# Optimization experiments

Hardware: AMD Instinct MI355X
Metric: run time of the kernel (lower is better)

Reference implementation:

```python
import jax, jax.numpy as jnp
import numpy as np

D_MODEL = 1024
N_HEADS = 16
D_K = D_MODEL // N_HEADS  # 64
D_FF = 2688
THETA = 10000.0
EPS = 1e-5
B, S = 2, 2048


def _rmsnorm(x, w):
    xf = x.astype(jnp.float32)
    ms = jnp.mean(xf * xf, axis=-1, keepdims=True)
    return (xf * w * jax.lax.rsqrt(ms + EPS)).astype(x.dtype)


def _rope(x, cos, sin):
    # x: [B, S, H, D_K]; cos/sin: [S, D_K//2]
    xe = x[..., 0::2]
    xo = x[..., 1::2]
    c = cos[None, :, None, :]
    s = sin[None, :, None, :]
    re = xe * c - xo * s
    ro = xe * s + xo * c
    # interleave back to even/odd layout
    return jnp.stack([re, ro], axis=-1).reshape(x.shape)


def setup_inputs() -> dict:
    key = jax.random.key(0)
    ks = jax.random.split(key, 12)
    sc = 0.02  # keep activations numerically sane (stand-in for trunc_normal init)
    return {
        "x": jax.random.normal(ks[0], (B, S, D_MODEL), dtype=jnp.float32),
        "ln1_w": jax.random.normal(ks[1], (D_MODEL,), dtype=jnp.float32) * sc + 1.0,
        "q_w": jax.random.normal(ks[2], (D_MODEL, D_MODEL), dtype=jnp.float32) * sc,
        "k_w": jax.random.normal(ks[3], (D_MODEL, D_MODEL), dtype=jnp.float32) * sc,
        "v_w": jax.random.normal(ks[4], (D_MODEL, D_MODEL), dtype=jnp.float32) * sc,
        "o_w": jax.random.normal(ks[5], (D_MODEL, D_MODEL), dtype=jnp.float32) * sc,
        "ln2_w": jax.random.normal(ks[6], (D_MODEL,), dtype=jnp.float32) * sc + 1.0,
        "w1_w": jax.random.normal(ks[7], (D_FF, D_MODEL), dtype=jnp.float32) * sc,
        "w3_w": jax.random.normal(ks[8], (D_FF, D_MODEL), dtype=jnp.float32) * sc,
        "w2_w": jax.random.normal(ks[9], (D_MODEL, D_FF), dtype=jnp.float32) * sc,
        "token_positions": jnp.arange(S, dtype=jnp.int32),
    }


def reference(x, ln1_w, q_w, k_w, v_w, o_w, ln2_w, w1_w, w3_w, w2_w, token_positions):
    b, s, _ = x.shape
    # --- pre-norm attention sublayer ---
    h = _rmsnorm(x, ln1_w)
    Q = (h @ q_w.T).reshape(b, s, N_HEADS, D_K)
    K = (h @ k_w.T).reshape(b, s, N_HEADS, D_K)
    V = (h @ v_w.T).reshape(b, s, N_HEADS, D_K)

    # RoPE tables from token positions
    pos = token_positions.astype(jnp.float32)                      # [S]
    kk = jnp.arange(D_K // 2, dtype=jnp.float32)
    inv_freq = THETA ** (-2.0 * kk / D_K)                          # [D_K/2]
    ang = pos[:, None] * inv_freq[None, :]                          # [S, D_K/2]
    cos, sin = jnp.cos(ang), jnp.sin(ang)

    Qr = _rope(Q, cos, sin)
    Kr = _rope(K, cos, sin)

    scale = 1.0 / jnp.sqrt(jnp.float32(D_K))
    scores = jnp.einsum("bqhd,bkhd->bhqk", Qr, Kr) * scale          # [B,H,S,S]
    causal = jnp.tril(jnp.ones((s, s), dtype=bool))
    scores = jnp.where(causal[None, None], scores, jnp.float32(-10000.0))
    attn = jax.nn.softmax(scores, axis=-1)
    ctx = jnp.einsum("bhqk,bkhd->bqhd", attn, V).reshape(b, s, D_MODEL)
    x1 = x + ctx @ o_w.T

    # --- pre-norm SwiGLU FFN sublayer ---
    h2 = _rmsnorm(x1, ln2_w)
    g = h2 @ w1_w.T                                                 # [B,S,D_FF]
    u = h2 @ w3_w.T
    ffn = (g * jax.nn.sigmoid(g) * u) @ w2_w.T
    return x1 + ffn
```

## Files before the change

kernel.cpp:

```cpp
#include <hip/hip_runtime.h>
#include <cstdint>

#define DM   1024
#define NH   16
#define DK   64
#define DFF  2688
#define SEQ  2048
#define BB   2
#define MTOT (BB*SEQ)

typedef __attribute__((ext_vector_type(8))) short short8;
typedef __attribute__((ext_vector_type(4))) float f32x4;

typedef const __attribute__((address_space(1))) void* gaddr_t;
typedef __attribute__((address_space(3))) void* laddr_t;
#define GLOAD_LDS16(g, l) __builtin_amdgcn_global_load_lds((gaddr_t)(g), (laddr_t)(l), 16, 0, 0)
#define MFMA16(a, b, c) __builtin_amdgcn_mfma_f32_16x16x32_bf16((a), (b), (c), 0, 0, 0)
#define WAIT_LDS() __builtin_amdgcn_s_waitcnt(0xc07f)

#define VMCNT(n) asm volatile("s_waitcnt vmcnt(" #n ")" ::: "memory")
#define BAR() do { asm volatile("" ::: "memory"); \
                   __builtin_amdgcn_s_barrier();  \
                   asm volatile("" ::: "memory"); } while (0)

__device__ __forceinline__ float bf2f(unsigned short u) {
    union { unsigned int i; float f; } v; v.i = ((unsigned int)u) << 16; return v.f;
}
__device__ __forceinline__ unsigned short f2bf(float f) {
    union { float f; unsigned int i; } v; v.f = f;
    unsigned int r = v.i + 0x7fffu + ((v.i >> 16) & 1u);
    return (unsigned short)(r >> 16);
}
__device__ __forceinline__ unsigned long long pack4bf(float a, float b, float c, float d) {
    return (unsigned long long)f2bf(a) | ((unsigned long long)f2bf(b) << 16)
         | ((unsigned long long)f2bf(c) << 32) | ((unsigned long long)f2bf(d) << 48);
}

__global__ __launch_bounds__(256)
void prep_k(const float* __restrict__ q_w, const float* __restrict__ k_w,
            const float* __restrict__ v_w, const float* __restrict__ o_w,
            const float* __restrict__ w1_w, const float* __restrict__ w3_w,
            const float* __restrict__ w2_w,
            unsigned short* __restrict__ Wqkv, unsigned short* __restrict__ Wo,
            unsigned short* __restrict__ W13, unsigned short* __restrict__ W2) {
    const int blk = blockIdx.x;
    const float* src; unsigned short* dst; int cols, rmul, roff, i;
    if (blk < 4096) {
        const int rr = blk >> 10;
        i = (blk & 1023) * 256 + threadIdx.x;
        cols = 1024; rmul = 1;
        if (rr == 0)      { src = q_w; dst = Wqkv; roff = 0; }
        else if (rr == 1) { src = k_w; dst = Wqkv; roff = 1024; }
        else if (rr == 2) { src = v_w; dst = Wqkv; roff = 2048; }
        else              { src = o_w; dst = Wo;   roff = 0; }
    } else if (blk < 6784) {
        i = (blk - 4096) * 256 + threadIdx.x; src = w1_w; dst = W13; cols = 1024; rmul = 2; roff = 0;
    } else if (blk < 9472) {
        i = (blk - 6784) * 256 + threadIdx.x; src = w3_w; dst = W13; cols = 1024; rmul = 2; roff = 1;
    } else {
        i = (blk - 9472) * 256 + threadIdx.x; src = w2_w; dst = W2;  cols = 2688; rmul = 1; roff = 0;
    }
    const int e = i * 4;
    const int r = e / cols, c = e - r * cols;
    const float4 v = *(const float4*)(src + e);
    ushort4 o;
    o.x = f2bf(v.x); o.y = f2bf(v.y); o.z = f2bf(v.z); o.w = f2bf(v.w);
    *(ushort4*)(dst + (size_t)(r * rmul + roff) * cols + c) = o;
}

__global__ __launch_bounds__(256)
void rmsnorm_k(const float* __restrict__ x, const float* __restrict__ w,
               unsigned short* __restrict__ out) {
    const int row = blockIdx.x;
    const int tid = threadIdx.x;
    const float4 v = ((const float4*)(x + (size_t)row * DM))[tid];
    float ss = v.x * v.x + v.y * v.y + v.z * v.z + v.w * v.w;
#pragma unroll
    for (int off = 32; off > 0; off >>= 1) ss += __shfl_down(ss, off, 64);
    __shared__ float sred[4];
    const int wave = tid >> 6, lane = tid & 63;
    if (lane == 0) sred[wave] = ss;
    __syncthreads();
    const float tot = sred[0] + sred[1] + sred[2] + sred[3];
    const float rinv = rsqrtf(tot * (1.0f / DM) + 1e-5f);
    const float4 wv = ((const float4*)w)[tid];
    ushort4 o;
    o.x = f2bf(v.x * wv.x * rinv);
    o.y = f2bf(v.y * wv.y * rinv);
    o.z = f2bf(v.z * wv.z * rinv);
    o.w = f2bf(v.w * wv.w * rinv);
    ((ushort4*)(out + (size_t)row * DM))[tid] = o;
}

__global__ void rope_tab_k(const int* __restrict__ pos, float* __restrict__ tab) {
    const int s = blockIdx.x, t = threadIdx.x;
    const int kk = t & 31;
    const float ang = (float)pos[s] * __expf(-0.28782313662f * (float)kk);
    tab[s * 64 + t] = (t < 32) ? cosf(ang) : sinf(ang);
}

template <int EPI>
__global__ __launch_bounds__(512)
void gemm_big(const unsigned short* __restrict__ A,
              const unsigned short* __restrict__ B,
              unsigned short* __restrict__ O0,
              unsigned short* __restrict__ O1,
              unsigned short* __restrict__ O2,
              const float* __restrict__ ROPT,
              int N, int K) {
    __shared__ unsigned short As[2][16384];
    __shared__ unsigned short Bs[2][8192];
    const int tid = threadIdx.x;
    const int wave = tid >> 6, lane = tid & 63;
    const int l15 = lane & 15, quad = lane >> 4;

    const int gx = gridDim.x;
    const int nwg = gx * gridDim.y;
    const int lin = blockIdx.y * gx + blockIdx.x;
    const int swz = (lin & 7) * (nwg >> 3) + (lin >> 3);
    const int bx = swz % gx, by = swz / gx;

    const int m0 = by * 256, n0 = bx * 128;
    const int wr = (wave >> 1) * 64, wc = (wave & 1) * 64;

    const f32x4 z4 = {0.f, 0.f, 0.f, 0.f};
    f32x4 acc[4][4];
#pragma unroll
    for (int i = 0; i < 4; i++)
#pragma unroll
        for (int j = 0; j < 4; j++) acc[i][j] = z4;

    const unsigned short* pa[4];
    const unsigned short* pb[2];
    int la[4], lb[2];
#pragma unroll
    for (int r = 0; r < 4; r++) {
        const int s = r * 512 + tid;
        pa[r] = A + (size_t)(m0 + (s & 255)) * K + (s >> 8) * 8;
        la[r] = (r * 512 + wave * 64) * 8;
    }
#pragma unroll
    for (int r = 0; r < 2; r++) {
        const int s = r * 512 + tid;
        pb[r] = B + (size_t)(n0 + (s & 127)) * K + (s >> 7) * 8;
        lb[r] = (r * 512 + wave * 64) * 8;
    }

    const int nt = K >> 6;

#pragma unroll
    for (int r = 0; r < 4; r++) { GLOAD_LDS16(pa[r], &As[0][la[r]]); pa[r] += 64; }
#pragma unroll
    for (int r = 0; r < 2; r++) { GLOAD_LDS16(pb[r], &Bs[0][lb[r]]); pb[r] += 64; }
    VMCNT(0);
    BAR();

    int cur = 0;
    for (int t = 0; t < nt; ++t) {
        if (t + 1 < nt) {
            const int nb = cur ^ 1;
#pragma unroll
            for (int r = 0; r < 4; r++) { GLOAD_LDS16(pa[r], &As[nb][la[r]]); pa[r] += 64; }
#pragma unroll
            for (int r = 0; r < 2; r++) { GLOAD_LDS16(pb[r], &Bs[nb][lb[r]]); pb[r] += 64; }
            VMCNT(6);
        } else {
            VMCNT(0);
        }
        BAR();
        __builtin_amdgcn_s_setprio(1);
#pragma unroll
        for (int kk = 0; kk < 2; kk++) {
            short8 af[4], bg[4];
#pragma unroll
            for (int tt = 0; tt < 4; tt++)
                af[tt] = *(const short8*)(&As[cur][((quad + 4 * kk) * 256 + wr + tt * 16 + l15) * 8]);
#pragma unroll
            for (int tt = 0; tt < 4; tt++)
                bg[tt] = *(const short8*)(&Bs[cur][((quad + 4 * kk) * 128 + wc + tt * 16 + l15) * 8]);
#pragma unroll
            for (int i = 0; i < 4; i++)
#pragma unroll
                for (int j = 0; j < 4; j++)
                    acc[i][j] = MFMA16(bg[j], af[i], acc[i][j]);
        }
        __builtin_amdgcn_s_setprio(0);
        BAR();
        cur ^= 1;
    }

#pragma unroll
    for (int i = 0; i < 4; i++) {
        const int r = m0 + wr + i * 16 + l15;
        if (EPI == 0) {
            const int b = r >> 11, s = r & (SEQ - 1);
            const float* rt = ROPT + s * 64;
#pragma unroll
            for (int j = 0; j < 4; j++) {
                const int cb = n0 + wc + j * 16;
                const int sec = cb >> 10;
                const int h = (cb & 1023) >> 6;
                const int cc0 = (cb & 63) + quad * 4;
                const f32x4 a = acc[i][j];
                if (sec < 2) {
                    const int p0 = cc0 >> 1;
                    const float cA = rt[p0],     sA = rt[32 + p0];
                    const float cB = rt[p0 + 1], sB = rt[32 + p0 + 1];
                    const float e0 = a[0] * cA - a[1] * sA;
                    const float o0 = a[0] * sA + a[1] * cA;
                    const float e1 = a[2] * cB - a[3] * sB;
                    const float o1 = a[2] * sB + a[3] * cB;
                    unsigned short* dst = (sec == 0) ? O0 : O1;
                    *(unsigned long long*)(dst + ((size_t)(b * NH + h) * SEQ + s) * DK + cc0) =
                        pack4bf(e0, o0, e1, o1);
                } else {
                    unsigned short* dst = O2 + ((size_t)(b * NH + h) * DK) * SEQ + s;
#pragma unroll
                    for (int t = 0; t < 4; t++)
                        dst[(size_t)(cc0 + t) * SEQ] = f2bf(a[t]);
                }
            }
        } else {
#pragma unroll
            for (int j = 0; j < 4; j++) {
                const int cc = n0 + wc + j * 16 + quad * 4;
                const f32x4 a = acc[i][j];
                const float s1 = a[0] * a[1] / (1.f + __expf(-a[0]));
                const float s2 = a[2] * a[3] / (1.f + __expf(-a[2]));
                *(unsigned int*)(O0 + (size_t)r * (DFF) + (cc >> 1)) =
                    (unsigned int)f2bf(s1) | ((unsigned int)f2bf(s2) << 16);
            }
        }
    }
}

__global__ __launch_bounds__(256, 4)
void gemm_thin(const unsigned short* __restrict__ A,
               const unsigned short* __restrict__ B,
               float* __restrict__ Cf,
               const float* __restrict__ R,
               int N, int K) {
    __shared__ unsigned short As[8192];
    __shared__ unsigned short Bs[4096];
    const int tid = threadIdx.x;
    const int wave = tid >> 6, lane = tid & 63;
    const int l15 = lane & 15, quad = lane >> 4;
    const int m0 = blockIdx.y * 128, n0 = blockIdx.x * 64;
    const int wr = (wave & 1) * 64, wc = (wave >> 1) * 32;

    const f32x4 z4 = {0.f, 0.f, 0.f, 0.f};
    f32x4 acc[4][2];
#pragma unroll
    for (int i = 0; i < 4; i++)
#pragma unroll
        for (int j = 0; j < 2; j++) acc[i][j] = z4;

    const unsigned short* ap[4];
    int al[4];
#pragma unroll
    for (int i = 0; i < 4; i++) {
        const int s = i * 256 + tid;
        ap[i] = A + (size_t)(m0 + (s & 127)) * K + (s >> 7) * 8;
        al[i] = (i * 256 + wave * 64) * 8;
    }
    const unsigned short* bp[2];
    int bl[2];
#pragma unroll
    for (int i = 0; i < 2; i++) {
        const int s = i * 256 + tid;
        bp[i] = B + (size_t)(n0 + (s & 63)) * K + (s >> 6) * 8;
        bl[i] = (i * 256 + wave * 64) * 8;
    }

    const int nk = K >> 6;
    for (int kc = 0; kc < nk; kc++) {
        __syncthreads();
#pragma unroll
        for (int i = 0; i < 4; i++) { GLOAD_LDS16(ap[i], &As[al[i]]); ap[i] += 64; }
#pragma unroll
        for (int i = 0; i < 2; i++) { GLOAD_LDS16(bp[i], &Bs[bl[i]]); bp[i] += 64; }
        __syncthreads();
#pragma unroll
        for (int h = 0; h < 2; h++) {
            short8 af[4], bg[2];
#pragma unroll
            for (int t = 0; t < 4; t++)
                af[t] = *(const short8*)(&As[((quad + 4 * h) * 128 + wr + t * 16 + l15) * 8]);
#pragma unroll
            for (int t = 0; t < 2; t++)
                bg[t] = *(const short8*)(&Bs[((quad + 4 * h) * 64 + wc + t * 16 + l15) * 8]);
#pragma unroll
            for (int i = 0; i < 4; i++)
#pragma unroll
                for (int j = 0; j < 2; j++)
                    acc[i][j] = MFMA16(bg[j], af[i], acc[i][j]);
        }
    }

#pragma unroll
    for (int i = 0; i < 4; i++) {
        const int r = m0 + wr + i * 16 + l15;
#pragma unroll
        for (int j = 0; j < 2; j++) {
            const int cc = n0 + wc + j * 16 + quad * 4;
            const size_t idx = (size_t)r * N + cc;
            const float4 rv = *(const float4*)(R + idx);
            float4 ov;
            ov.x = acc[i][j][0] + rv.x;
            ov.y = acc[i][j][1] + rv.y;
            ov.z = acc[i][j][2] + rv.z;
            ov.w = acc[i][j][3] + rv.w;
            *(float4*)(Cf + idx) = ov;
        }
    }
}

template <bool MASK>
__device__ __forceinline__ void softmax_tile(f32x4 st[4], float& li, unsigned short* Pw,
                                             int l15, int quad, int j0, int myq) {
    float lsum = 0.f;
#pragma unroll
    for (int t = 0; t < 4; t++) {
#pragma unroll
        for (int r = 0; r < 4; r++) {
            float v = st[t][r] * 0.125f;
            if (MASK) {
                const int key = j0 + t * 16 + quad * 4 + r;
                if (key > myq) v = -1e30f;
            }
            const float p = __expf(v);
            st[t][r] = p;
            lsum += p;
        }
        *(unsigned long long*)(Pw + l15 * 72 + t * 16 + quad * 4) =
            pack4bf(st[t][0], st[t][1], st[t][2], st[t][3]);
    }
    li += lsum;
}

__global__ __launch_bounds__(256, 2)
void attn_k(const unsigned short* __restrict__ Qr, const unsigned short* __restrict__ Kr,
            const unsigned short* __restrict__ Vt, unsigned short* __restrict__ ctx) {
    __shared__ unsigned short KVl[2][8192];
    __shared__ unsigned short Pl[4 * 2 * 1152];
    const int tid = threadIdx.x;
    const int wave = tid >> 6, lane = tid & 63;
    const int l15 = lane & 15, quad = lane >> 4;
    const int bh = blockIdx.y, b = bh >> 4, h = bh & 15;
    const int g = blockIdx.x;
    const int qtA = g * 4 + wave, qtB = 127 - qtA;
    const int q0A = qtA * 16, q0B = qtB * 16;
    const int countA = g + 1, countB = 32 - g;
    const unsigned short* Kb = Kr + (size_t)bh * SEQ * DK;
    const unsigned short* Vb = Vt + (size_t)bh * DK * SEQ;

    const unsigned short* QbA = Qr + ((size_t)bh * SEQ + q0A) * DK;
    const unsigned short* QbB = Qr + ((size_t)bh * SEQ + q0B) * DK;
    const short8 qfA0 = *(const short8*)(QbA + l15 * DK + quad * 8);
    const short8 qfA1 = *(const short8*)(QbA + l15 * DK + 32 + quad * 8);
    const short8 qfB0 = *(const short8*)(QbB + l15 * DK + quad * 8);
    const short8 qfB1 = *(const short8*)(QbB + l15 * DK + 32 + quad * 8);

    const int slot0 = wave * 128 + lane, slot1 = slot0 + 64;
    const int ck0 = slot0 >> 3, s0 = slot0 & 7;
    const int ck1 = slot1 >> 3, s1 = slot1 & 7;
    const unsigned short* kp0 = Kb + ck0 * 64 + (s0 ^ (ck0 & 7)) * 8;
    const unsigned short* kp1 = Kb + ck1 * 64 + (s1 ^ (ck1 & 7)) * 8;
    const unsigned short* vp0 = Vb + ck0 * 2048 + (s0 ^ (ck0 & 7)) * 8;
    const unsigned short* vp1 = Vb + ck1 * 2048 + (s1 ^ (ck1 & 7)) * 8;
    const int kb0 = wave * 1024, kb1 = kb0 + 512;

    unsigned short* PA = Pl + (wave * 2 + 0) * 1152;
    unsigned short* PB = Pl + (wave * 2 + 1) * 1152;

    const f32x4 z4 = {0.f, 0.f, 0.f, 0.f};
    f32x4 oA[4], oB[4];
#pragma unroll
    for (int d = 0; d < 4; d++) { oA[d] = z4; oB[d] = z4; }
    float liA = 0.f, liB = 0.f;
    const int myqA = q0A + l15, myqB = q0B + l15;
    const int xr = l15 & 7;

    GLOAD_LDS16(kp0, &KVl[0][kb0]);
    GLOAD_LDS16(kp1, &KVl[0][kb1]);
    GLOAD_LDS16(vp0, &KVl[0][4096 + kb0]);
    GLOAD_LDS16(vp1, &KVl[0][4096 + kb1]);
    kp0 += 4096; kp1 += 4096; vp0 += 64; vp1 += 64;

    for (int j = 0; j < countB; ++j) {
        const int bf = j & 1;
        const unsigned short* Kl = KVl[bf];
        const unsigned short* Vl = KVl[bf] + 4096;
        __syncthreads();
        if (j + 1 < countB) {
            GLOAD_LDS16(kp0, &KVl[bf ^ 1][kb0]);
            GLOAD_LDS16(kp1, &KVl[bf ^ 1][kb1]);
            GLOAD_LDS16(vp0, &KVl[bf ^ 1][4096 + kb0]);
            GLOAD_LDS16(vp1, &KVl[bf ^ 1][4096 + kb1]);
            kp0 += 4096; kp1 += 4096; vp0 += 64; vp1 += 64;
        }
        const int j0 = j * 64;
        short8 kf[4][2];
#pragma unroll
        for (int t = 0; t < 4; t++) {
            const unsigned short* kr = Kl + (t * 16 + l15) * 64;
            kf[t][0] = *(const short8*)(kr + (quad ^ xr) * 8);
            kf[t][1] = *(const short8*)(kr + ((4 + quad) ^ xr) * 8);
        }
        f32x4 stB[4];
#pragma unroll
        for (int t = 0; t < 4; t++)
            stB[t] = MFMA16(kf[t][1], qfB1, MFMA16(kf[t][0], qfB0, z4));
        const bool doA = (j < countA);
        if (doA) {
            f32x4 stA[4];
#pragma unroll
            for (int t = 0; t < 4; t++)
                stA[t] = MFMA16(kf[t][1], qfA1, MFMA16(kf[t][0], qfA0, z4));
            if (j == countA - 1) softmax_tile<true >(stA, liA, PA, l15, quad, j0, myqA);
            else                 softmax_tile<false>(stA, liA, PA, l15, quad, j0, myqA);
        }
        if (j == countB - 1) softmax_tile<true >(stB, liB, PB, l15, quad, j0, myqB);
        else                 softmax_tile<false>(stB, liB, PB, l15, quad, j0, myqB);
        WAIT_LDS();
        short8 vf[4][2];
#pragma unroll
        for (int dt = 0; dt < 4; dt++) {
            const unsigned short* vr = Vl + (dt * 16 + l15) * 64;
            vf[dt][0] = *(const short8*)(vr + (quad ^ xr) * 8);
            vf[dt][1] = *(const short8*)(vr + ((4 + quad) ^ xr) * 8);
        }
        {
            const short8 pfB0 = *(const short8*)(PB + l15 * 72 + quad * 8);
            const short8 pfB1 = *(const short8*)(PB + l15 * 72 + 32 + quad * 8);
#pragma unroll
            for (int dt = 0; dt < 4; dt++)
                oB[dt] = MFMA16(vf[dt][1], pfB1, MFMA16(vf[dt][0], pfB0, oB[dt]));
        }
        if (doA) {
            const short8 pfA0 = *(const short8*)(PA + l15 * 72 + quad * 8);
            const short8 pfA1 = *(const short8*)(PA + l15 * 72 + 32 + quad * 8);
#pragma unroll
            for (int dt = 0; dt < 4; dt++)
                oA[dt] = MFMA16(vf[dt][1], pfA1, MFMA16(vf[dt][0], pfA0, oA[dt]));
        }
    }
    liA += __shfl_xor(liA, 16, 64); liA += __shfl_xor(liA, 32, 64);
    liB += __shfl_xor(liB, 16, 64); liB += __shfl_xor(liB, 32, 64);
    const float invA = 1.0f / liA, invB = 1.0f / liB;
#pragma unroll
    for (int dt = 0; dt < 4; dt++) {
        *(unsigned long long*)(PA + l15 * 72 + dt * 16 + quad * 4) =
            pack4bf(oA[dt][0] * invA, oA[dt][1] * invA, oA[dt][2] * invA, oA[dt][3] * invA);
        *(unsigned long long*)(PB + l15 * 72 + dt * 16 + quad * 4) =
            pack4bf(oB[dt][0] * invB, oB[dt][1] * invB, oB[dt][2] * invB, oB[dt][3] * invB);
    }
    WAIT_LDS();
    const int row = lane >> 2, seg = (lane & 3) * 8;
#pragma unroll
    for (int p = 0; p < 2; p++) {
        const int cs = seg + p * 32;
        const uint4 va = *(const uint4*)(PA + row * 72 + cs);
        *(uint4*)(ctx + ((size_t)b * SEQ + q0A + row) * DM + h * DK + cs) = va;
        const uint4 vb = *(const uint4*)(PB + row * 72 + cs);
        *(uint4*)(ctx + ((size_t)b * SEQ + q0B + row) * DM + h * DK + cs) = vb;
    }
}

extern "C" void kernel_launch(void* const* d_in, const int* in_sizes, int n_in,
                              void* d_out, int out_size, void* d_ws, size_t ws_size,
                              hipStream_t stream) {
    const float* x     = (const float*)d_in[0];
    const float* ln1_w = (const float*)d_in[1];
    const float* q_w   = (const float*)d_in[2];
    const float* k_w   = (const float*)d_in[3];
    const float* v_w   = (const float*)d_in[4];
    const float* o_w   = (const float*)d_in[5];
    const float* ln2_w = (const float*)d_in[6];
    const float* w1_w  = (const float*)d_in[7];
    const float* w3_w  = (const float*)d_in[8];
    const float* w2_w  = (const float*)d_in[9];
    const int*   tpos  = (const int*)d_in[10];
    float* out = (float*)d_out;
    char* ws = (char*)d_ws;

    unsigned short* Wqkv = (unsigned short*)(ws + 0);
    unsigned short* Wo   = (unsigned short*)(ws + 6291456);
    unsigned short* W13  = (unsigned short*)(ws + 8388608);
    unsigned short* W2   = (unsigned short*)(ws + 19398656);
    float*          X1   = (float*)(ws + 24903680);
    float*          ROPT = (float*)(ws + 24903680);
    char* base = ws + 41680896;
    unsigned short* H    = (unsigned short*)(base);
    unsigned short* QR   = (unsigned short*)(base + 8388608);
    unsigned short* KR   = (unsigned short*)(base + 16777216);
    unsigned short* VT   = (unsigned short*)(base + 25165824);
    unsigned short* CTX  = (unsigned short*)(base + 33554432);
    unsigned short* H2   = (unsigned short*)(base);
    unsigned short* ACT  = (unsigned short*)(base + 41943040);

    prep_k<<<12160, 256, 0, stream>>>(q_w, k_w, v_w, o_w, w1_w, w3_w, w2_w,
                                      Wqkv, Wo, W13, W2);
    rope_tab_k<<<2048, 64, 0, stream>>>(tpos, ROPT);

    rmsnorm_k<<<4096, 256, 0, stream>>>(x, ln1_w, H);
    gemm_big<0><<<dim3(24, 16), 512, 0, stream>>>(H, Wqkv, QR, KR, VT, ROPT, 3072, 1024);
    attn_k<<<dim3(16, 32), 256, 0, stream>>>(QR, KR, VT, CTX);
    gemm_thin<<<dim3(16, 32), 256, 0, stream>>>(CTX, Wo, X1, x, 1024, 1024);
    rmsnorm_k<<<4096, 256, 0, stream>>>(X1, ln2_w, H2);
    gemm_big<1><<<dim3(42, 16), 512, 0, stream>>>(H2, W13, ACT, nullptr, nullptr, nullptr, 5376, 1024);
    gemm_thin<<<dim3(16, 32), 256, 0, stream>>>(ACT, W2, out, X1, 1024, 2688);
}
```

Before: 480.1 us.

## Widen big GEMM tile to 256x192 with staged B prefetch and band swizzle

```diff
diff --git a/kernel.cpp b/kernel.cpp
--- a/kernel.cpp
+++ b/kernel.cpp
@@ -34,6 +34,14 @@
 __device__ __forceinline__ unsigned long long pack4bf(float a, float b, float c, float d) {
     return (unsigned long long)f2bf(a) | ((unsigned long long)f2bf(b) << 16)
          | ((unsigned long long)f2bf(c) << 32) | ((unsigned long long)f2bf(d) << 48);
+}
+
+__device__ __forceinline__ void band_swizzle(int& bx, int& by) {
+    const int gx = gridDim.x;
+    const int lin = blockIdx.y * gx + blockIdx.x;
+    const int xcd = lin & 7, k = lin >> 3;
+    by = xcd * 4 + (k & 3);
+    bx = k >> 2;
 }
 
 __global__ __launch_bounds__(256)
@@ -101,15 +109,15 @@
 
 template <int EPI>
 __global__ __launch_bounds__(512)
-void gemm_big(const unsigned short* __restrict__ A,
-              const unsigned short* __restrict__ B,
-              unsigned short* __restrict__ O0,
-              unsigned short* __restrict__ O1,
-              unsigned short* __restrict__ O2,
-              const float* __restrict__ ROPT,
-              int N, int K) {
+void gemm256(const unsigned short* __restrict__ A,
+             const unsigned short* __restrict__ B,
+             unsigned short* __restrict__ O0,
+             unsigned short* __restrict__ O1,
+             unsigned short* __restrict__ O2,
+             const float* __restrict__ ROPT,
+             int N, int K) {
     __shared__ unsigned short As[2][16384];
-    __shared__ unsigned short Bs[2][8192];
+    __shared__ unsigned short Bs[2][12288];
     const int tid = threadIdx.x;
     const int wave = tid >> 6, lane = tid & 63;
     const int l15 = lane & 15, quad = lane >> 4;
@@ -119,30 +127,31 @@
     const int lin = blockIdx.y * gx + blockIdx.x;
     const int swz = (lin & 7) * (nwg >> 3) + (lin >> 3);
     const int bx = swz % gx, by = swz / gx;
-
-    const int m0 = by * 256, n0 = bx * 128;
-    const int wr = (wave >> 1) * 64, wc = (wave & 1) * 64;
+    const int m0 = by * 256, n0 = bx * 192;
+    const int wr = (wave >> 2) * 128, wc = (wave & 3) * 48;
 
     const f32x4 z4 = {0.f, 0.f, 0.f, 0.f};
-    f32x4 acc[4][4];
-#pragma unroll
-    for (int i = 0; i < 4; i++)
-#pragma unroll
-        for (int j = 0; j < 4; j++) acc[i][j] = z4;
+    f32x4 acc[8][3];
+#pragma unroll
+    for (int m = 0; m < 8; m++)
+#pragma unroll
+        for (int n = 0; n < 3; n++) acc[m][n] = z4;
 
     const unsigned short* pa[4];
-    const unsigned short* pb[2];
-    int la[4], lb[2];
+    int la[4];
 #pragma unroll
     for (int r = 0; r < 4; r++) {
         const int s = r * 512 + tid;
         pa[r] = A + (size_t)(m0 + (s & 255)) * K + (s >> 8) * 8;
         la[r] = (r * 512 + wave * 64) * 8;
     }
-#pragma unroll
-    for (int r = 0; r < 2; r++) {
+    const unsigned short* pb[3];
+    int lb[3];
+#pragma unroll
+    for (int r = 0; r < 3; r++) {
         const int s = r * 512 + tid;
-        pb[r] = B + (size_t)(n0 + (s & 127)) * K + (s >> 7) * 8;
+        const int bk = s / 192, br = s - bk * 192;
+        pb[r] = B + (size_t)(n0 + br) * K + bk * 8;
         lb[r] = (r * 512 + wave * 64) * 8;
     }
 
@@ -151,57 +160,66 @@
 #pragma unroll
     for (int r = 0; r < 4; r++) { GLOAD_LDS16(pa[r], &As[0][la[r]]); pa[r] += 64; }
 #pragma unroll
-    for (int r = 0; r < 2; r++) { GLOAD_LDS16(pb[r], &Bs[0][lb[r]]); pb[r] += 64; }
-    VMCNT(0);
-    BAR();
+    for (int r = 0; r < 3; r++) { GLOAD_LDS16(pb[r], &Bs[0][lb[r]]); pb[r] += 64; }
 
     int cur = 0;
     for (int t = 0; t < nt; ++t) {
+        const int nb = cur ^ 1;
         if (t + 1 < nt) {
-            const int nb = cur ^ 1;
 #pragma unroll
             for (int r = 0; r < 4; r++) { GLOAD_LDS16(pa[r], &As[nb][la[r]]); pa[r] += 64; }
-#pragma unroll
-            for (int r = 0; r < 2; r++) { GLOAD_LDS16(pb[r], &Bs[nb][lb[r]]); pb[r] += 64; }
-            VMCNT(6);
+            VMCNT(4);
         } else {
             VMCNT(0);
         }
         BAR();
-        __builtin_amdgcn_s_setprio(1);
-#pragma unroll
-        for (int kk = 0; kk < 2; kk++) {
-            short8 af[4], bg[4];
-#pragma unroll
-            for (int tt = 0; tt < 4; tt++)
-                af[tt] = *(const short8*)(&As[cur][((quad + 4 * kk) * 256 + wr + tt * 16 + l15) * 8]);
-#pragma unroll
-            for (int tt = 0; tt < 4; tt++)
-                bg[tt] = *(const short8*)(&Bs[cur][((quad + 4 * kk) * 128 + wc + tt * 16 + l15) * 8]);
-#pragma unroll
-            for (int i = 0; i < 4; i++)
-#pragma unroll
-                for (int j = 0; j < 4; j++)
-                    acc[i][j] = MFMA16(bg[j], af[i], acc[i][j]);
-        }
-        __builtin_amdgcn_s_setprio(0);
-        BAR();
-        cur ^= 1;
-    }
-
-#pragma unroll
-    for (int i = 0; i < 4; i++) {
-        const int r = m0 + wr + i * 16 + l15;
+
+        short8 bg[3][2];
+#pragma unroll
+        for (int n = 0; n < 3; n++)
+#pragma unroll
+            for (int kk = 0; kk < 2; kk++)
+                bg[n][kk] = *(const short8*)(&Bs[cur][((quad + 4 * kk) * 192 + wc + n * 16 + l15) * 8]);
+
+#pragma unroll
+        for (int p = 0; p < 4; ++p) {
+            if (p == 1 && t + 1 < nt) {
+#pragma unroll
+                for (int r = 0; r < 3; r++) { GLOAD_LDS16(pb[r], &Bs[nb][lb[r]]); pb[r] += 64; }
+            }
+            short8 af[2][2];
+#pragma unroll
+            for (int m = 0; m < 2; m++)
+#pragma unroll
+                for (int kk = 0; kk < 2; kk++)
+                    af[m][kk] = *(const short8*)(&As[cur][((quad + 4 * kk) * 256 + wr + (p * 2 + m) * 16 + l15) * 8]);
+            __builtin_amdgcn_s_setprio(1);
+#pragma unroll
+            for (int m = 0; m < 2; m++)
+#pragma unroll
+                for (int n = 0; n < 3; n++)
+#pragma unroll
+                    for (int kk = 0; kk < 2; kk++)
+                        acc[p * 2 + m][n] = MFMA16(bg[n][kk], af[m][kk], acc[p * 2 + m][n]);
+            __builtin_amdgcn_s_setprio(0);
+            BAR();
+        }
+        cur = nb;
+    }
+
+#pragma unroll
+    for (int m = 0; m < 8; m++) {
+        const int r = m0 + wr + m * 16 + l15;
         if (EPI == 0) {
             const int b = r >> 11, s = r & (SEQ - 1);
             const float* rt = ROPT + s * 64;
 #pragma unroll
-            for (int j = 0; j < 4; j++) {
-                const int cb = n0 + wc + j * 16;
+            for (int n = 0; n < 3; n++) {
+                const int cb = n0 + wc + n * 16;
                 const int sec = cb >> 10;
                 const int h = (cb & 1023) >> 6;
                 const int cc0 = (cb & 63) + quad * 4;
-                const f32x4 a = acc[i][j];
+                const f32x4 a = acc[m][n];
                 if (sec < 2) {
                     const int p0 = cc0 >> 1;
                     const float cA = rt[p0],     sA = rt[32 + p0];
@@ -216,15 +234,15 @@
                 } else {
                     unsigned short* dst = O2 + ((size_t)(b * NH + h) * DK) * SEQ + s;
 #pragma unroll
-                    for (int t = 0; t < 4; t++)
-                        dst[(size_t)(cc0 + t) * SEQ] = f2bf(a[t]);
+                    for (int tq = 0; tq < 4; tq++)
+                        dst[(size_t)(cc0 + tq) * SEQ] = f2bf(a[tq]);
                 }
             }
         } else {
 #pragma unroll
-            for (int j = 0; j < 4; j++) {
-                const int cc = n0 + wc + j * 16 + quad * 4;
-                const f32x4 a = acc[i][j];
+            for (int n = 0; n < 3; n++) {
+                const int cc = n0 + wc + n * 16 + quad * 4;
+                const f32x4 a = acc[m][n];
                 const float s1 = a[0] * a[1] / (1.f + __expf(-a[0]));
                 const float s2 = a[2] * a[3] / (1.f + __expf(-a[2]));
                 *(unsigned int*)(O0 + (size_t)r * (DFF) + (cc >> 1)) =
@@ -245,7 +263,9 @@
     const int tid = threadIdx.x;
     const int wave = tid >> 6, lane = tid & 63;
     const int l15 = lane & 15, quad = lane >> 4;
-    const int m0 = blockIdx.y * 128, n0 = blockIdx.x * 64;
+    int bx, by;
+    band_swizzle(bx, by);
+    const int m0 = by * 128, n0 = bx * 64;
     const int wr = (wave & 1) * 64, wc = (wave >> 1) * 32;
 
     const f32x4 z4 = {0.f, 0.f, 0.f, 0.f};
@@ -504,10 +524,10 @@
     rope_tab_k<<<2048, 64, 0, stream>>>(tpos, ROPT);
 
     rmsnorm_k<<<4096, 256, 0, stream>>>(x, ln1_w, H);
-    gemm_big<0><<<dim3(24, 16), 512, 0, stream>>>(H, Wqkv, QR, KR, VT, ROPT, 3072, 1024);
+    gemm256<0><<<dim3(16, 16), 512, 0, stream>>>(H, Wqkv, QR, KR, VT, ROPT, 3072, 1024);
     attn_k<<<dim3(16, 32), 256, 0, stream>>>(QR, KR, VT, CTX);
     gemm_thin<<<dim3(16, 32), 256, 0, stream>>>(CTX, Wo, X1, x, 1024, 1024);
     rmsnorm_k<<<4096, 256, 0, stream>>>(X1, ln2_w, H2);
-    gemm_big<1><<<dim3(42, 16), 512, 0, stream>>>(H2, W13, ACT, nullptr, nullptr, nullptr, 5376, 1024);
+    gemm256<1><<<dim3(28, 16), 512, 0, stream>>>(H2, W13, ACT, nullptr, nullptr, nullptr, 5376, 1024);
     gemm_thin<<<dim3(16, 32), 256, 0, stream>>>(ACT, W2, out, X1, 1024, 2688);
 }
```

Result: faster. 411.5 us (-14.3%).
